# Kernel tuning notes

Measured on AMD Instinct MI355X. Metric: run time of the kernel, lower is better.

The kernel has to match this reference:

```python
import jax, jax.numpy as jnp
import numpy as np

B, N, DIM, EMB_H, EXP, K = 1, 1024, 64, 64, 4, 16


def setup_inputs() -> dict:
    key = jax.random.key(0)
    ks = jax.random.split(key, 12)
    s = lambda k, *shape: jax.random.normal(k, shape, dtype=jnp.float32) * 0.05
    return {
        "x": jax.random.normal(ks[0], (B, N, DIM), dtype=jnp.float32),
        "pos": jax.random.normal(ks[1], (B, N, 3), dtype=jnp.float32),
        "Wq": s(ks[2], DIM, DIM),
        "Wk": s(ks[3], DIM, DIM),
        "Wv": s(ks[4], DIM, DIM),
        "P1": s(ks[5], 3, EMB_H), "pb1": jnp.zeros((EMB_H,), jnp.float32),
        "P2": s(ks[6], EMB_H, DIM), "pb2": jnp.zeros((DIM,), jnp.float32),
        "A1": s(ks[7], DIM, DIM * EXP), "ab1": jnp.zeros((DIM * EXP,), jnp.float32),
        "A2": s(ks[8], DIM * EXP, DIM), "ab2": jnp.zeros((DIM,), jnp.float32),
        "nneighbors": K,
    }


def reference(x, pos, Wq, Wk, Wv, P1, pb1, P2, pb2, A1, ab1, A2, ab2, nneighbors):
    b, n, d = x.shape
    q = x @ Wq            # [b,n,d]
    k = x @ Wk
    v = x @ Wv
    qk_rel = q[:, :, None, :] - k[:, None, :, :]          # [b,n,n,d]
    rel_pos = pos[:, :, None, :] - pos[:, None, :, :]      # [b,n,n,3]
    rel_pos_emb = jax.nn.relu(rel_pos @ P1 + pb1) @ P2 + pb2  # [b,n,n,d]
    # kNN selection on euclidean distance (smallest nneighbors)
    rel_dist = jnp.linalg.norm(rel_pos, axis=-1)           # [b,n,n]
    _, idx = jax.lax.top_k(-rel_dist, nneighbors)          # [b,n,K]
    bidx = jnp.arange(b)[:, None, None]
    v_g = v[bidx, idx]                                     # [b,n,K,d]
    qk_g = jnp.take_along_axis(qk_rel, idx[..., None], axis=2)        # [b,n,K,d]
    rpe_g = jnp.take_along_axis(rel_pos_emb, idx[..., None], axis=2)  # [b,n,K,d]
    v_g = v_g + rpe_g
    sim = jax.nn.relu((qk_g + rpe_g) @ A1 + ab1) @ A2 + ab2  # [b,n,K,d]
    attn = jax.nn.softmax(sim, axis=-2)                      # softmax over neighbors
    agg = jnp.sum(attn * v_g, axis=2)                        # [b,n,d]
    return agg
```

## Files before the change

### kernel.cpp

```cpp
#include <hip/hip_runtime.h>
#include <climits>

#define NPTS 1024
#define DIMD 64
#define KNN  16
#define HID  256
#define EMBH 64

typedef short short8 __attribute__((ext_vector_type(8)));
typedef float f32x4  __attribute__((ext_vector_type(4)));

__device__ __forceinline__ short f2bf(float x) {
    unsigned u = __float_as_uint(x);
    unsigned r = (u + 0x7fffu + ((u >> 16) & 1u)) >> 16;
    return (short)r;
}
__device__ __forceinline__ float bf2f(short s) {
    return __uint_as_float(((unsigned)(unsigned short)s) << 16);
}

#define AOFF(k, m) ((((k) >> 3) * 16 + (m)) * 8 + ((k) & 7))

__device__ __host__ __forceinline__ int frag_off(int K, int k, int n) {
    int T = n >> 4, c = k >> 5, q = (k >> 3) & 3, j = k & 7;
    int lane = (q << 4) | (n & 15);
    return ((T * (K >> 5) + c) * 64 + lane) * 8 + j;
}

#define A1H 0
#define A2H 16384
#define WKH 32768
#define WVH 36864
#define P2H 40960

__global__ __launch_bounds__(256) void prep_weights(
    const float* __restrict__ A1, const float* __restrict__ A2,
    const float* __restrict__ Wk, const float* __restrict__ Wv,
    const float* __restrict__ P2, short* __restrict__ ws)
{
    int e = blockIdx.x * 256 + threadIdx.x;
    float v; int base, off;
    if (e < 16384)      { int k = e >> 8, n = e & 255;               v = A1[e];
                          base = A1H; off = frag_off(64,  k, n); }
    else if (e < 32768) { int t = e - 16384; int k = t >> 6, n = t & 63; v = A2[t];
                          base = A2H; off = frag_off(256, k, n); }
    else if (e < 36864) { int t = e - 32768; int k = t >> 6, n = t & 63; v = Wk[t];
                          base = WKH; off = frag_off(64,  k, n); }
    else if (e < 40960) { int t = e - 36864; int k = t >> 6, n = t & 63; v = Wv[t];
                          base = WVH; off = frag_off(64,  k, n); }
    else if (e < 45056) { int t = e - 40960; int k = t >> 6, n = t & 63; v = P2[t];
                          base = P2H; off = frag_off(64,  k, n); }
    else return;
    ws[base + off] = f2bf(v);
}

__global__ __launch_bounds__(256, 4) void ptl_fused(
    const float* __restrict__ x,  const float* __restrict__ pos,
    const float* __restrict__ Wq,
    const float* __restrict__ P1, const float* __restrict__ pb1,
    const float* __restrict__ pb2,
    const float* __restrict__ ab1, const float* __restrict__ ab2,
    const short* __restrict__ ws,
    float* __restrict__ out)
{
    __shared__ __align__(16) short a_xn_hi[16*64],  a_xn_lo[16*64];
    __shared__ __align__(16) short a_es_hi[16*64],  a_es_lo[16*64];
    __shared__ __align__(16) short a_h_hi [16*64],  a_h_lo [16*64];
    __shared__ __align__(16) short a_hd_hi[16*256], a_hd_lo[16*256];
    __shared__ __align__(16) float s_vg[16*68];
    __shared__ __align__(16) float s_sim[16*68];
    __shared__ float s_q[DIMD];
    __shared__ int   s_idx[KNN];
    __shared__ int   s_cnt, s_cnt2, s_need;
    __shared__ unsigned s_pref;

    const int i    = blockIdx.x;
    const int tid  = threadIdx.x;
    const int lane = tid & 63;
    const int w    = tid >> 6;
    const int q4   = lane >> 4;
    const int col  = lane & 15;

    const float px = pos[i*3+0], py = pos[i*3+1], pz = pos[i*3+2];

    unsigned ku[4];
    #pragma unroll
    for (int u = 0; u < 4; u++) {
        int j = tid + 256 * u;
        float dx = __fsub_rn(px, pos[j*3+0]);
        float dy = __fsub_rn(py, pos[j*3+1]);
        float dz = __fsub_rn(pz, pos[j*3+2]);
        float s  = __fadd_rn(__fadd_rn(__fmul_rn(dx,dx), __fmul_rn(dy,dy)), __fmul_rn(dz,dz));
        ku[u] = __float_as_uint(__fsqrt_rn(s));
    }

    int* histI = (int*)a_hd_hi;
    int* s_tie = (int*)a_hd_lo;
    if (tid == 0) { s_cnt = 0; s_cnt2 = 0; s_pref = 0u; s_need = KNN; }

    for (int r = 0; r < 4; r++) {
        const int shift = 24 - 8 * r;
        for (int t = tid; t < 4 * 257; t += 256) histI[t] = 0;
        __syncthreads();
        unsigned pref = s_pref;
        #pragma unroll
        for (int u = 0; u < 4; u++) {
            unsigned k = ku[u];
            bool match = true;
            if (r > 0) match = ((k >> (shift + 8)) == (pref >> (shift + 8)));
            if (match) atomicAdd(&histI[w * 257 + ((k >> shift) & 255)], 1);
        }
        __syncthreads();
        if (w == 0) {
            int b0 = lane * 4, cnt4[4], loc = 0;
            #pragma unroll
            for (int t = 0; t < 4; t++) {
                int s = 0;
                #pragma unroll
                for (int ww = 0; ww < 4; ww++) s += histI[ww * 257 + b0 + t];
                cnt4[t] = s; loc += s;
            }
            int incl = loc;
            #pragma unroll
            for (int off = 1; off < 64; off <<= 1) {
                int t = __shfl_up(incl, off);
                if (lane >= off) incl += t;
            }
            int excl = incl - loc;
            int need = s_need;
            unsigned long long mk = __ballot(incl >= need);
            int lstar = (int)__ffsll((long long)mk) - 1;
            if (lane == lstar) {
                int run = excl, t = 0;
                while (t < 3 && run + cnt4[t] < need) { run += cnt4[t]; t++; }
                s_pref = pref | ((unsigned)(b0 + t) << shift);
                s_need = need - run;
            }
        }
        __syncthreads();
    }
    const unsigned T = s_pref;
    const int needT  = s_need;

    #pragma unroll
    for (int u = 0; u < 4; u++) {
        unsigned k = ku[u];
        int j = tid + 256 * u;
        if (k < T)       { int p = atomicAdd(&s_cnt, 1);  s_idx[p] = j; }
        else if (k == T) { int p = atomicAdd(&s_cnt2, 1); if (p < 256) s_tie[p] = j; }
    }
    __syncthreads();

    if (w == 0) {
        int base = s_cnt;
        int m = s_cnt2;
        if (m == needT) {
            for (int t = lane; t < m; t += 64) s_idx[base + t] = s_tie[t];
        } else {
            int cand[4];
            #pragma unroll
            for (int t = 0; t < 4; t++) {
                int e = lane + 64 * t;
                cand[t] = (e < m && e < 256) ? s_tie[e] : INT_MAX;
            }
            for (int sel = 0; sel < needT; sel++) {
                int mv = cand[0];
                #pragma unroll
                for (int t = 1; t < 4; t++) mv = min(mv, cand[t]);
                #pragma unroll
                for (int off = 32; off > 0; off >>= 1) mv = min(mv, __shfl_xor(mv, off));
                #pragma unroll
                for (int t = 0; t < 4; t++) if (cand[t] == mv) cand[t] = INT_MAX;
                if (lane == 0) s_idx[base + sel] = mv;
            }
        }
    } else if (w == 1) {
        int d = lane;
        const float4* xr = (const float4*)(x + i * DIMD);
        float aq = 0.f;
        #pragma unroll
        for (int cb = 0; cb < DIMD / 4; cb++) {
            float4 xv = xr[cb];
            const float* wq = Wq + (cb*4) * DIMD + d;
            aq = fmaf(xv.x, wq[0*DIMD], aq); aq = fmaf(xv.y, wq[1*DIMD], aq);
            aq = fmaf(xv.z, wq[2*DIMD], aq); aq = fmaf(xv.w, wq[3*DIMD], aq);
        }
        s_q[d] = aq;
    }
    __syncthreads();

    #pragma unroll
    for (int u = 0; u < 4; u++) {
        int t = tid + 256 * u;
        int kk = t >> 6, c = t & 63;
        int j = s_idx[kk];
        int ao = AOFF(c, kk);
        float xv = x[j * DIMD + c];
        short xh = f2bf(xv);
        a_xn_hi[ao] = xh;
        a_xn_lo[ao] = f2bf(xv - bf2f(xh));
        float dx = px - pos[j*3+0];
        float dy = py - pos[j*3+1];
        float dz = pz - pos[j*3+2];
        float a = pb1[c];
        a = fmaf(dx, P1[0*EMBH+c], a);
        a = fmaf(dy, P1[1*EMBH+c], a);
        a = fmaf(dz, P1[2*EMBH+c], a);
        a = fmaxf(a, 0.0f);
        short eh = f2bf(a);
        a_es_hi[ao] = eh;
        a_es_lo[ao] = f2bf(a - bf2f(eh));
    }
    __syncthreads();

    const short8* wsv  = (const short8*)ws;
    const short8* xnh  = (const short8*)a_xn_hi;
    const short8* xnl  = (const short8*)a_xn_lo;
    const short8* esh  = (const short8*)a_es_hi;
    const short8* esl  = (const short8*)a_es_lo;
    const short8* hhv  = (const short8*)a_h_hi;
    const short8* hlv  = (const short8*)a_h_lo;
    const short8* hdh  = (const short8*)a_hd_hi;
    const short8* hdl  = (const short8*)a_hd_lo;

    auto bfrag = [&](int short_base, int f) -> short8 {
        return wsv[(short_base >> 3) + f * 64 + lane];
    };

    {
        f32x4 acck = {0,0,0,0}, accv = {0,0,0,0}, accr = {0,0,0,0};
        #pragma unroll
        for (int c = 0; c < 2; c++) {
            int av = (4*c + q4) * 16 + col;
            short8 xh = xnh[av], xl = xnl[av];
            int f = w * 2 + c;
            short8 bk = bfrag(WKH, f);
            short8 bv = bfrag(WVH, f);
            acck = __builtin_amdgcn_mfma_f32_16x16x32_bf16(xh, bk, acck, 0,0,0);
            acck = __builtin_amdgcn_mfma_f32_16x16x32_bf16(xl, bk, acck, 0,0,0);
            accv = __builtin_amdgcn_mfma_f32_16x16x32_bf16(xh, bv, accv, 0,0,0);
            accv = __builtin_amdgcn_mfma_f32_16x16x32_bf16(xl, bv, accv, 0,0,0);
        }
        #pragma unroll
        for (int c = 0; c < 2; c++) {
            int av = (4*c + q4) * 16 + col;
            short8 eh = esh[av], el = esl[av];
            short8 bp = bfrag(P2H, w * 2 + c);
            accr = __builtin_amdgcn_mfma_f32_16x16x32_bf16(eh, bp, accr, 0,0,0);
            accr = __builtin_amdgcn_mfma_f32_16x16x32_bf16(el, bp, accr, 0,0,0);
        }
        int d = w * 16 + col;
        float qd = s_q[d], pb = pb2[d];
        #pragma unroll
        for (int r = 0; r < 4; r++) {
            int s = q4 * 4 + r;
            float rpe = accr[r] + pb;
            float hv  = qd - acck[r] + rpe;
            s_vg[s * 68 + d] = accv[r] + rpe;
            int ao = AOFF(d, s);
            short hh = f2bf(hv);
            a_h_hi[ao] = hh;
            a_h_lo[ao] = f2bf(hv - bf2f(hh));
        }
    }
    __syncthreads();

    {
        short8 hh[2], hl[2];
        #pragma unroll
        for (int c = 0; c < 2; c++) {
            int av = (4*c + q4) * 16 + col;
            hh[c] = hhv[av]; hl[c] = hlv[av];
        }
        #pragma unroll
        for (int t = 0; t < 4; t++) {
            int T4 = w * 4 + t;
            f32x4 acc = {0,0,0,0};
            #pragma unroll
            for (int c = 0; c < 2; c++) {
                short8 bh = bfrag(A1H, T4 * 2 + c);
                acc = __builtin_amdgcn_mfma_f32_16x16x32_bf16(hh[c], bh, acc, 0,0,0);
                acc = __builtin_amdgcn_mfma_f32_16x16x32_bf16(hl[c], bh, acc, 0,0,0);
            }
            int n = T4 * 16 + col;
            float bias = ab1[n];
            #pragma unroll
            for (int r = 0; r < 4; r++) {
                float val = fmaxf(acc[r] + bias, 0.0f);
                int ao = AOFF(n, q4 * 4 + r);
                short vh = f2bf(val);
                a_hd_hi[ao] = vh;
                a_hd_lo[ao] = f2bf(val - bf2f(vh));
            }
        }
    }
    __syncthreads();

    {
        f32x4 acc0 = {0,0,0,0}, acc1 = {0,0,0,0};
        #pragma unroll
        for (int c = 0; c < 8; c += 2) {
            {
                int av = (4*c + q4) * 16 + col;
                short8 ah = hdh[av], al = hdl[av];
                short8 bh = bfrag(A2H, w * 8 + c);
                acc0 = __builtin_amdgcn_mfma_f32_16x16x32_bf16(ah, bh, acc0, 0,0,0);
                acc0 = __builtin_amdgcn_mfma_f32_16x16x32_bf16(al, bh, acc0, 0,0,0);
            }
            {
                int av = (4*(c+1) + q4) * 16 + col;
                short8 ah = hdh[av], al = hdl[av];
                short8 bh = bfrag(A2H, w * 8 + c + 1);
                acc1 = __builtin_amdgcn_mfma_f32_16x16x32_bf16(ah, bh, acc1, 0,0,0);
                acc1 = __builtin_amdgcn_mfma_f32_16x16x32_bf16(al, bh, acc1, 0,0,0);
            }
        }
        int n = w * 16 + col;
        float bias = ab2[n];
        #pragma unroll
        for (int r = 0; r < 4; r++)
            s_sim[(q4 * 4 + r) * 68 + n] = acc0[r] + acc1[r] + bias;
    }
    __syncthreads();

    if (tid < DIMD) {
        int d = tid;
        float mx = -3.0e38f;
        #pragma unroll
        for (int kk = 0; kk < KNN; kk++) mx = fmaxf(mx, s_sim[kk * 68 + d]);
        float den = 0.0f, num = 0.0f;
        #pragma unroll
        for (int kk = 0; kk < KNN; kk++) {
            float e = expf(s_sim[kk * 68 + d] - mx);
            den += e;
            num = fmaf(e, s_vg[kk * 68 + d], num);
        }
        out[i * DIMD + d] = num / den;
    }
}

extern "C" void kernel_launch(void* const* d_in, const int* in_sizes, int n_in,
                              void* d_out, int out_size, void* d_ws, size_t ws_size,
                              hipStream_t stream) {
    const float* x   = (const float*)d_in[0];
    const float* pos = (const float*)d_in[1];
    const float* Wq  = (const float*)d_in[2];
    const float* Wk  = (const float*)d_in[3];
    const float* Wv  = (const float*)d_in[4];
    const float* P1  = (const float*)d_in[5];
    const float* pb1 = (const float*)d_in[6];
    const float* P2  = (const float*)d_in[7];
    const float* pb2 = (const float*)d_in[8];
    const float* A1  = (const float*)d_in[9];
    const float* ab1 = (const float*)d_in[10];
    const float* A2  = (const float*)d_in[11];
    const float* ab2 = (const float*)d_in[12];
    float* out = (float*)d_out;
    short* ws  = (short*)d_ws;

    prep_weights<<<(45056 + 255) / 256, 256, 0, stream>>>(A1, A2, Wk, Wv, P2, ws);
    ptl_fused<<<NPTS, 256, 0, stream>>>(x, pos, Wq, P1, pb1, pb2, ab1, ab2, ws, out);
}
```

Before: 95.97 us.

## Process two query points per block with two waves each; vectorize weight prep

The fused kernel now handles two query points per 256-thread block. Each point gets 128 threads (two waves) and its own shared-memory region, laid out as a manually aliased buffer, so the grid is halved. Each wave now computes more MFMA tiles per stage, which cuts per-block overhead and lets weight fragments be shared across points through the cache. The weight-prep kernel writes whole short8 fragments per thread instead of scattering single elements. The trade-offs are more work serialized per wave, more registers, and fewer blocks to hide latency.

```diff
diff --git a/kernel.cpp b/kernel.cpp
--- a/kernel.cpp
+++ b/kernel.cpp
@@ -20,12 +20,6 @@
 }
 
 #define AOFF(k, m) ((((k) >> 3) * 16 + (m)) * 8 + ((k) & 7))
-
-__device__ __host__ __forceinline__ int frag_off(int K, int k, int n) {
-    int T = n >> 4, c = k >> 5, q = (k >> 3) & 3, j = k & 7;
-    int lane = (q << 4) | (n & 15);
-    return ((T * (K >> 5) + c) * 64 + lane) * 8 + j;
-}
 
 #define A1H 0
 #define A2H 16384
@@ -39,20 +33,40 @@
     const float* __restrict__ P2, short* __restrict__ ws)
 {
     int e = blockIdx.x * 256 + threadIdx.x;
-    float v; int base, off;
-    if (e < 16384)      { int k = e >> 8, n = e & 255;               v = A1[e];
-                          base = A1H; off = frag_off(64,  k, n); }
-    else if (e < 32768) { int t = e - 16384; int k = t >> 6, n = t & 63; v = A2[t];
-                          base = A2H; off = frag_off(256, k, n); }
-    else if (e < 36864) { int t = e - 32768; int k = t >> 6, n = t & 63; v = Wk[t];
-                          base = WKH; off = frag_off(64,  k, n); }
-    else if (e < 40960) { int t = e - 36864; int k = t >> 6, n = t & 63; v = Wv[t];
-                          base = WVH; off = frag_off(64,  k, n); }
-    else if (e < 45056) { int t = e - 40960; int k = t >> 6, n = t & 63; v = P2[t];
-                          base = P2H; off = frag_off(64,  k, n); }
-    else return;
-    ws[base + off] = f2bf(v);
-}
+    if (e >= 88 * 64) return;
+    int f = e >> 6, lane = e & 63;
+    int q = (lane >> 4) & 3, nn = lane & 15;
+    const float* src; int N, base, lf, cpt;
+    if (f < 32)      { src = A1; N = 256; base = A1H; lf = f;      cpt = 2; }
+    else if (f < 64) { src = A2; N = 64;  base = A2H; lf = f - 32; cpt = 8; }
+    else if (f < 72) { src = Wk; N = 64;  base = WKH; lf = f - 64; cpt = 2; }
+    else if (f < 80) { src = Wv; N = 64;  base = WVH; lf = f - 72; cpt = 2; }
+    else             { src = P2; N = 64;  base = P2H; lf = f - 80; cpt = 2; }
+    int T = lf / cpt, c = lf % cpt;
+    int n  = T * 16 + nn;
+    int k0 = c * 32 + q * 8;
+    short8 v;
+    #pragma unroll
+    for (int j = 0; j < 8; j++) v[j] = f2bf(src[(k0 + j) * N + n]);
+    *(short8*)(ws + base + lf * 512 + lane * 8) = v;
+}
+
+#define PT_STRIDE 29568
+#define S_XN_HI 0
+#define S_XN_LO 1024
+#define S_ES_HI 2048
+#define S_ES_LO 3072
+#define S_H_HI  4096
+#define S_H_LO  5120
+#define S_HD_HI 0
+#define S_HD_LO 6144
+#define I_HIST  3072
+#define I_TIE   2048
+#define I_IDX   7360
+#define I_CTRL  7376
+#define F_VG    5120
+#define F_SIM   6208
+#define F_Q     7296
 
 __global__ __launch_bounds__(256, 4) void ptl_fused(
     const float* __restrict__ x,  const float* __restrict__ pos,
@@ -63,30 +77,29 @@
     const short* __restrict__ ws,
     float* __restrict__ out)
 {
-    __shared__ __align__(16) short a_xn_hi[16*64],  a_xn_lo[16*64];
-    __shared__ __align__(16) short a_es_hi[16*64],  a_es_lo[16*64];
-    __shared__ __align__(16) short a_h_hi [16*64],  a_h_lo [16*64];
-    __shared__ __align__(16) short a_hd_hi[16*256], a_hd_lo[16*256];
-    __shared__ __align__(16) float s_vg[16*68];
-    __shared__ __align__(16) float s_sim[16*68];
-    __shared__ float s_q[DIMD];
-    __shared__ int   s_idx[KNN];
-    __shared__ int   s_cnt, s_cnt2, s_need;
-    __shared__ unsigned s_pref;
-
-    const int i    = blockIdx.x;
+    __shared__ __align__(16) char smem[2 * PT_STRIDE];
+
     const int tid  = threadIdx.x;
     const int lane = tid & 63;
     const int w    = tid >> 6;
+    const int h    = w & 1;
+    const int p    = tid >> 7;
+    const int tl   = tid & 127;
     const int q4   = lane >> 4;
     const int col  = lane & 15;
 
-    const float px = pos[i*3+0], py = pos[i*3+1], pz = pos[i*3+2];
-
-    unsigned ku[4];
-    #pragma unroll
-    for (int u = 0; u < 4; u++) {
-        int j = tid + 256 * u;
+    char* bptr = smem + p * PT_STRIDE;
+    short* sS = (short*)bptr;
+    float* sF = (float*)bptr;
+    int*   sI = (int*)bptr;
+
+    const int ip = blockIdx.x * 2 + p;
+    const float px = pos[ip*3+0], py = pos[ip*3+1], pz = pos[ip*3+2];
+
+    unsigned ku[8];
+    #pragma unroll
+    for (int u = 0; u < 8; u++) {
+        int j = tl + 128 * u;
         float dx = __fsub_rn(px, pos[j*3+0]);
         float dy = __fsub_rn(py, pos[j*3+1]);
         float dz = __fsub_rn(pz, pos[j*3+2]);
@@ -94,30 +107,27 @@
         ku[u] = __float_as_uint(__fsqrt_rn(s));
     }
 
-    int* histI = (int*)a_hd_hi;
-    int* s_tie = (int*)a_hd_lo;
-    if (tid == 0) { s_cnt = 0; s_cnt2 = 0; s_pref = 0u; s_need = KNN; }
+    int* hist = sI + I_HIST;
+    int* ctrl = sI + I_CTRL;
+    if (tl == 0) { ctrl[0] = 0; ctrl[1] = 0; ctrl[2] = KNN; ctrl[3] = 0; }
 
     for (int r = 0; r < 4; r++) {
         const int shift = 24 - 8 * r;
-        for (int t = tid; t < 4 * 257; t += 256) histI[t] = 0;
+        for (int t = tl; t < 2 * 257; t += 128) hist[t] = 0;
         __syncthreads();
-        unsigned pref = s_pref;
-        #pragma unroll
-        for (int u = 0; u < 4; u++) {
+        unsigned pref = (unsigned)ctrl[3];
+        #pragma unroll
+        for (int u = 0; u < 8; u++) {
             unsigned k = ku[u];
-            bool match = true;
-            if (r > 0) match = ((k >> (shift + 8)) == (pref >> (shift + 8)));
-            if (match) atomicAdd(&histI[w * 257 + ((k >> shift) & 255)], 1);
+            bool match = (r == 0) || ((k >> (shift + 8)) == (pref >> (shift + 8)));
+            if (match) atomicAdd(&hist[h * 257 + ((k >> shift) & 255)], 1);
         }
         __syncthreads();
-        if (w == 0) {
+        if (h == 0) {
             int b0 = lane * 4, cnt4[4], loc = 0;
             #pragma unroll
             for (int t = 0; t < 4; t++) {
-                int s = 0;
-                #pragma unroll
-                for (int ww = 0; ww < 4; ww++) s += histI[ww * 257 + b0 + t];
+                int s = hist[b0 + t] + hist[257 + b0 + t];
                 cnt4[t] = s; loc += s;
             }
             int incl = loc;
@@ -127,41 +137,43 @@
                 if (lane >= off) incl += t;
             }
             int excl = incl - loc;
-            int need = s_need;
+            int need = ctrl[2];
             unsigned long long mk = __ballot(incl >= need);
             int lstar = (int)__ffsll((long long)mk) - 1;
             if (lane == lstar) {
                 int run = excl, t = 0;
                 while (t < 3 && run + cnt4[t] < need) { run += cnt4[t]; t++; }
-                s_pref = pref | ((unsigned)(b0 + t) << shift);
-                s_need = need - run;
+                ctrl[3] = (int)(pref | ((unsigned)(b0 + t) << shift));
+                ctrl[2] = need - run;
             }
         }
         __syncthreads();
     }
-    const unsigned T = s_pref;
-    const int needT  = s_need;
-
-    #pragma unroll
-    for (int u = 0; u < 4; u++) {
+    const unsigned T = (unsigned)ctrl[3];
+    const int needT  = ctrl[2];
+
+    int* tie = sI + I_TIE;
+    int* idx = sI + I_IDX;
+    #pragma unroll
+    for (int u = 0; u < 8; u++) {
         unsigned k = ku[u];
-        int j = tid + 256 * u;
-        if (k < T)       { int p = atomicAdd(&s_cnt, 1);  s_idx[p] = j; }
-        else if (k == T) { int p = atomicAdd(&s_cnt2, 1); if (p < 256) s_tie[p] = j; }
-    }
-    __syncthreads();
-
-    if (w == 0) {
-        int base = s_cnt;
-        int m = s_cnt2;
+        int j = tl + 128 * u;
+        if (k < T)       { int pp = atomicAdd(&ctrl[0], 1); idx[pp] = j; }
+        else if (k == T) { int pp = atomicAdd(&ctrl[1], 1); if (pp < 256) tie[pp] = j; }
+    }
+    __syncthreads();
+
+    if (h == 0) {
+        int base = ctrl[0];
+        int m = ctrl[1];
         if (m == needT) {
-            for (int t = lane; t < m; t += 64) s_idx[base + t] = s_tie[t];
+            for (int t = lane; t < m; t += 64) idx[base + t] = tie[t];
         } else {
             int cand[4];
             #pragma unroll
             for (int t = 0; t < 4; t++) {
                 int e = lane + 64 * t;
-                cand[t] = (e < m && e < 256) ? s_tie[e] : INT_MAX;
+                cand[t] = (e < m && e < 256) ? tie[e] : INT_MAX;
             }
             for (int sel = 0; sel < needT; sel++) {
                 int mv = cand[0];
@@ -171,12 +183,12 @@
                 for (int off = 32; off > 0; off >>= 1) mv = min(mv, __shfl_xor(mv, off));
                 #pragma unroll
                 for (int t = 0; t < 4; t++) if (cand[t] == mv) cand[t] = INT_MAX;
-                if (lane == 0) s_idx[base + sel] = mv;
-            }
-        }
-    } else if (w == 1) {
+                if (lane == 0) idx[base + sel] = mv;
+            }
+        }
+    } else {
         int d = lane;
-        const float4* xr = (const float4*)(x + i * DIMD);
+        const float4* xr = (const float4*)(x + ip * DIMD);
         float aq = 0.f;
         #pragma unroll
         for (int cb = 0; cb < DIMD / 4; cb++) {
@@ -185,20 +197,20 @@
             aq = fmaf(xv.x, wq[0*DIMD], aq); aq = fmaf(xv.y, wq[1*DIMD], aq);
             aq = fmaf(xv.z, wq[2*DIMD], aq); aq = fmaf(xv.w, wq[3*DIMD], aq);
         }
-        s_q[d] = aq;
-    }
-    __syncthreads();
-
-    #pragma unroll
-    for (int u = 0; u < 4; u++) {
-        int t = tid + 256 * u;
+        sF[F_Q + d] = aq;
+    }
+    __syncthreads();
+
+    #pragma unroll
+    for (int u = 0; u < 8; u++) {
+        int t = tl + 128 * u;
         int kk = t >> 6, c = t & 63;
-        int j = s_idx[kk];
+        int j = idx[kk];
         int ao = AOFF(c, kk);
         float xv = x[j * DIMD + c];
         short xh = f2bf(xv);
-        a_xn_hi[ao] = xh;
-        a_xn_lo[ao] = f2bf(xv - bf2f(xh));
+        sS[S_XN_HI + ao] = xh;
+        sS[S_XN_LO + ao] = f2bf(xv - bf2f(xh));
         float dx = px - pos[j*3+0];
         float dy = py - pos[j*3+1];
         float dz = pz - pos[j*3+2];
@@ -208,59 +220,75 @@
         a = fmaf(dz, P1[2*EMBH+c], a);
         a = fmaxf(a, 0.0f);
         short eh = f2bf(a);
-        a_es_hi[ao] = eh;
-        a_es_lo[ao] = f2bf(a - bf2f(eh));
-    }
-    __syncthreads();
-
-    const short8* wsv  = (const short8*)ws;
-    const short8* xnh  = (const short8*)a_xn_hi;
-    const short8* xnl  = (const short8*)a_xn_lo;
-    const short8* esh  = (const short8*)a_es_hi;
-    const short8* esl  = (const short8*)a_es_lo;
-    const short8* hhv  = (const short8*)a_h_hi;
-    const short8* hlv  = (const short8*)a_h_lo;
-    const short8* hdh  = (const short8*)a_hd_hi;
-    const short8* hdl  = (const short8*)a_hd_lo;
-
+        sS[S_ES_HI + ao] = eh;
+        sS[S_ES_LO + ao] = f2bf(a - bf2f(eh));
+    }
+    __syncthreads();
+
+    const short8* wsv = (const short8*)ws;
     auto bfrag = [&](int short_base, int f) -> short8 {
         return wsv[(short_base >> 3) + f * 64 + lane];
     };
+    const short8* xnh = (const short8*)(sS + S_XN_HI);
+    const short8* xnl = (const short8*)(sS + S_XN_LO);
+    const short8* esh = (const short8*)(sS + S_ES_HI);
+    const short8* esl = (const short8*)(sS + S_ES_LO);
+    const short8* hhv = (const short8*)(sS + S_H_HI);
+    const short8* hlv = (const short8*)(sS + S_H_LO);
+    const short8* hdh = (const short8*)(sS + S_HD_HI);
+    const short8* hdl = (const short8*)(sS + S_HD_LO);
 
     {
-        f32x4 acck = {0,0,0,0}, accv = {0,0,0,0}, accr = {0,0,0,0};
+        short8 xh[2], xl[2], eh[2], el[2];
         #pragma unroll
         for (int c = 0; c < 2; c++) {
             int av = (4*c + q4) * 16 + col;
-            short8 xh = xnh[av], xl = xnl[av];
-            int f = w * 2 + c;
-            short8 bk = bfrag(WKH, f);
-            short8 bv = bfrag(WVH, f);
-            acck = __builtin_amdgcn_mfma_f32_16x16x32_bf16(xh, bk, acck, 0,0,0);
-            acck = __builtin_amdgcn_mfma_f32_16x16x32_bf16(xl, bk, acck, 0,0,0);
-            accv = __builtin_amdgcn_mfma_f32_16x16x32_bf16(xh, bv, accv, 0,0,0);
-            accv = __builtin_amdgcn_mfma_f32_16x16x32_bf16(xl, bv, accv, 0,0,0);
-        }
-        #pragma unroll
-        for (int c = 0; c < 2; c++) {
-            int av = (4*c + q4) * 16 + col;
-            short8 eh = esh[av], el = esl[av];
-            short8 bp = bfrag(P2H, w * 2 + c);
-            accr = __builtin_amdgcn_mfma_f32_16x16x32_bf16(eh, bp, accr, 0,0,0);
-            accr = __builtin_amdgcn_mfma_f32_16x16x32_bf16(el, bp, accr, 0,0,0);
-        }
-        int d = w * 16 + col;
-        float qd = s_q[d], pb = pb2[d];
-        #pragma unroll
-        for (int r = 0; r < 4; r++) {
-            int s = q4 * 4 + r;
-            float rpe = accr[r] + pb;
-            float hv  = qd - acck[r] + rpe;
-            s_vg[s * 68 + d] = accv[r] + rpe;
-            int ao = AOFF(d, s);
-            short hh = f2bf(hv);
-            a_h_hi[ao] = hh;
-            a_h_lo[ao] = f2bf(hv - bf2f(hh));
+            xh[c] = xnh[av]; xl[c] = xnl[av];
+            eh[c] = esh[av]; el[c] = esl[av];
+        }
+        f32x4 acck[2], accv[2], accr[2];
+        #pragma unroll
+        for (int T2 = 0; T2 < 2; T2++) {
+            int Tt = h * 2 + T2;
+            f32x4 ak = {0,0,0,0}, av_ = {0,0,0,0}, ar = {0,0,0,0};
+            #pragma unroll
+            for (int c = 0; c < 2; c++) {
+                int f = Tt * 2 + c;
+                short8 bk = bfrag(WKH, f);
+                ak = __builtin_amdgcn_mfma_f32_16x16x32_bf16(xh[c], bk, ak, 0,0,0);
+                ak = __builtin_amdgcn_mfma_f32_16x16x32_bf16(xl[c], bk, ak, 0,0,0);
+            }
+            #pragma unroll
+            for (int c = 0; c < 2; c++) {
+                int f = Tt * 2 + c;
+                short8 bv = bfrag(WVH, f);
+                av_ = __builtin_amdgcn_mfma_f32_16x16x32_bf16(xh[c], bv, av_, 0,0,0);
+                av_ = __builtin_amdgcn_mfma_f32_16x16x32_bf16(xl[c], bv, av_, 0,0,0);
+            }
+            #pragma unroll
+            for (int c = 0; c < 2; c++) {
+                int f = Tt * 2 + c;
+                short8 bp = bfrag(P2H, f);
+                ar = __builtin_amdgcn_mfma_f32_16x16x32_bf16(eh[c], bp, ar, 0,0,0);
+                ar = __builtin_amdgcn_mfma_f32_16x16x32_bf16(el[c], bp, ar, 0,0,0);
+            }
+            acck[T2] = ak; accv[T2] = av_; accr[T2] = ar;
+        }
+        #pragma unroll
+        for (int T2 = 0; T2 < 2; T2++) {
+            int d = (h * 2 + T2) * 16 + col;
+            float qd = sF[F_Q + d], pb = pb2[d];
+            #pragma unroll
+            for (int r = 0; r < 4; r++) {
+                int s = q4 * 4 + r;
+                float rpe = accr[T2][r] + pb;
+                float hv  = qd - acck[T2][r] + rpe;
+                sF[F_VG + s * 68 + d] = accv[T2][r] + rpe;
+                int ao = AOFF(d, s);
+                short hh = f2bf(hv);
+                sS[S_H_HI + ao] = hh;
+                sS[S_H_LO + ao] = f2bf(hv - bf2f(hh));
+            }
         }
     }
     __syncthreads();
@@ -273,69 +301,62 @@
             hh[c] = hhv[av]; hl[c] = hlv[av];
         }
         #pragma unroll
-        for (int t = 0; t < 4; t++) {
-            int T4 = w * 4 + t;
+        for (int t = 0; t < 8; t++) {
+            int Tt = h * 8 + t;
             f32x4 acc = {0,0,0,0};
             #pragma unroll
             for (int c = 0; c < 2; c++) {
-                short8 bh = bfrag(A1H, T4 * 2 + c);
+                short8 bh = bfrag(A1H, Tt * 2 + c);
                 acc = __builtin_amdgcn_mfma_f32_16x16x32_bf16(hh[c], bh, acc, 0,0,0);
                 acc = __builtin_amdgcn_mfma_f32_16x16x32_bf16(hl[c], bh, acc, 0,0,0);
             }
-            int n = T4 * 16 + col;
+            int n = Tt * 16 + col;
             float bias = ab1[n];
             #pragma unroll
             for (int r = 0; r < 4; r++) {
                 float val = fmaxf(acc[r] + bias, 0.0f);
                 int ao = AOFF(n, q4 * 4 + r);
                 short vh = f2bf(val);
-                a_hd_hi[ao] = vh;
-                a_hd_lo[ao] = f2bf(val - bf2f(vh));
-            }
-        }
-    }
-    __syncthreads();
-
-    {
-        f32x4 acc0 = {0,0,0,0}, acc1 = {0,0,0,0};
-        #pragma unroll
-        for (int c = 0; c < 8; c += 2) {
-            {
-                int av = (4*c + q4) * 16 + col;
-                short8 ah = hdh[av], al = hdl[av];
-                short8 bh = bfrag(A2H, w * 8 + c);
-                acc0 = __builtin_amdgcn_mfma_f32_16x16x32_bf16(ah, bh, acc0, 0,0,0);
-                acc0 = __builtin_amdgcn_mfma_f32_16x16x32_bf16(al, bh, acc0, 0,0,0);
-            }
-            {
-                int av = (4*(c+1) + q4) * 16 + col;
-                short8 ah = hdh[av], al = hdl[av];
-                short8 bh = bfrag(A2H, w * 8 + c + 1);
-                acc1 = __builtin_amdgcn_mfma_f32_16x16x32_bf16(ah, bh, acc1, 0,0,0);
-                acc1 = __builtin_amdgcn_mfma_f32_16x16x32_bf16(al, bh, acc1, 0,0,0);
-            }
-        }
-        int n = w * 16 + col;
+                sS[S_HD_HI + ao] = vh;
+                sS[S_HD_LO + ao] = f2bf(val - bf2f(vh));
+            }
+        }
+    }
+    __syncthreads();
+
+    #pragma unroll
+    for (int T2 = 0; T2 < 2; T2++) {
+        int Tt = h * 2 + T2;
+        f32x4 acc = {0,0,0,0};
+        #pragma unroll
+        for (int c = 0; c < 8; c++) {
+            int av = (4*c + q4) * 16 + col;
+            short8 ah = hdh[av], al = hdl[av];
+            short8 bh = bfrag(A2H, Tt * 8 + c);
+            acc = __builtin_amdgcn_mfma_f32_16x16x32_bf16(ah, bh, acc, 0,0,0);
+            acc = __builtin_amdgcn_mfma_f32_16x16x32_bf16(al, bh, acc, 0,0,0);
+        }
+        int n = Tt * 16 + col;
         float bias = ab2[n];
         #pragma unroll
         for (int r = 0; r < 4; r++)
-            s_sim[(q4 * 4 + r) * 68 + n] = acc0[r] + acc1[r] + bias;
-    }
-    __syncthreads();
-
-    if (tid < DIMD) {
-        int d = tid;
+            sF[F_SIM + (q4 * 4 + r) * 68 + n] = acc[r] + bias;
+    }
+    __syncthreads();
+
+    if (tl < DIMD) {
+        int d = tl;
         float mx = -3.0e38f;
         #pragma unroll
-        for (int kk = 0; kk < KNN; kk++) mx = fmaxf(mx, s_sim[kk * 68 + d]);
+        for (int kk = 0; kk < KNN; kk++) mx = fmaxf(mx, sF[F_SIM + kk * 68 + d]);
         float den = 0.0f, num = 0.0f;
         #pragma unroll
         for (int kk = 0; kk < KNN; kk++) {
-            float e = expf(s_sim[kk * 68 + d] - mx);
+            float e = expf(sF[F_SIM + kk * 68 + d] - mx);
             den += e;
-            num = fmaf(e, s_vg[kk * 68 + d], num);
-        }
-        out[i * DIMD + d] = num / den;
+            num = fmaf(e, sF[F_VG + kk * 68 + d], num);
+        }
+        out[ip * DIMD + d] = num / den;
     }
 }
 
@@ -358,6 +379,6 @@
     float* out = (float*)d_out;
     short* ws  = (short*)d_ws;
 
-    prep_weights<<<(45056 + 255) / 256, 256, 0, stream>>>(A1, A2, Wk, Wv, P2, ws);
-    ptl_fused<<<NPTS, 256, 0, stream>>>(x, pos, Wq, P1, pb1, pb2, ab1, ab2, ws, out);
-}
+    prep_weights<<<22, 256, 0, stream>>>(A1, A2, Wk, Wv, P2, ws);
+    ptl_fused<<<NPTS / 2, 256, 0, stream>>>(x, pos, Wq, P1, pb1, pb2, ab1, ab2, ws, out);
+}
```

After: 96.52 us. About the same (+0.6%).
